# Performance work log

Hardware: AMD Instinct MI355X
Metric: run time of the kernel (lower is better)

The kernel has to match this reference:

```python
import jax, jax.numpy as jnp
import numpy as np

NUM_HEADS = 16
ROPE_BASE = 10000.0
MAX_POS = 4096


def _rope_tables(head_dim):
    inv_freq = 1.0 / (ROPE_BASE ** (np.arange(0, head_dim, 2, dtype=np.float32) / head_dim))
    freqs = np.arange(MAX_POS, dtype=np.float32)[:, None] * inv_freq[None, :]
    emb = np.concatenate([freqs, freqs], axis=-1)  # [MAX_POS, head_dim]
    return jnp.asarray(np.cos(emb)), jnp.asarray(np.sin(emb))


def _rotate_half(x):
    d = x.shape[-1] // 2
    return jnp.concatenate([-x[..., d:], x[..., :d]], axis=-1)


def _apply_rope(x, pos, cos_t, sin_t):
    # x: [B,H,S,D], pos: [B,S]
    cos = cos_t[pos][:, None]  # [B,1,S,D]
    sin = sin_t[pos][:, None]
    return x * cos + _rotate_half(x) * sin


def setup_inputs() -> dict:
    key = jax.random.key(0)
    ks = jax.random.split(key, 8)
    B, N, M, C = 2, 2048, 2048, 1024
    s = 1.0 / np.sqrt(C)
    return {
        "query": jax.random.normal(ks[0], (B, N, C), jnp.float32),
        "key": jax.random.normal(ks[1], (B, M, C), jnp.float32),
        "query_pos": jnp.broadcast_to(jnp.arange(N, dtype=jnp.int32), (B, N)),
        "key_pos": jnp.broadcast_to(jnp.arange(M, dtype=jnp.int32), (B, M)),
        "Wq": jax.random.normal(ks[2], (C, C), jnp.float32) * s,
        "bq": jnp.zeros((C,), jnp.float32),
        "Wk": jax.random.normal(ks[3], (C, C), jnp.float32) * s,
        "Wv": jax.random.normal(ks[4], (C, C), jnp.float32) * s,
        "bv": jnp.zeros((C,), jnp.float32),
        "Wo": jax.random.normal(ks[5], (C, C), jnp.float32) * s,
        "bo": jnp.zeros((C,), jnp.float32),
    }


def reference(query, key, query_pos, key_pos, Wq, bq, Wk, Wv, bv, Wo, bo):
    B, N, C = query.shape
    M = key.shape[1]
    H = NUM_HEADS
    D = C // H
    scale = D ** -0.5
    cos_t, sin_t = _rope_tables(D)

    value = key  # value defaults to key
    identity = query

    q = (query @ Wq.T + bq).reshape(B, N, H, D).transpose(0, 2, 1, 3)
    k = (key @ Wk.T).reshape(B, M, H, D).transpose(0, 2, 1, 3)
    v = (value @ Wv.T + bv).reshape(B, M, H, D).transpose(0, 2, 1, 3)

    q = _apply_rope(q, query_pos, cos_t, sin_t)
    k = _apply_rope(k, key_pos, cos_t, sin_t)

    attn = jnp.einsum('bhnd,bhmd->bhnm', q, k) * scale
    attn = jax.nn.softmax(attn, axis=-1)
    x = jnp.einsum('bhnm,bhmd->bhnd', attn, v)  # [B,H,N,D]
    x = x.transpose(0, 2, 1, 3).reshape(B, N, C)
    x = x @ Wo.T + bo
    return x + identity
```

## Files before the change

### kernel.cpp

```cpp
#include <hip/hip_runtime.h>
#include <hip/hip_bf16.h>
#include <stdint.h>

#define B_ 2
#define N_ 2048
#define M_ 2048
#define C_ 1024
#define H_ 16
#define D_ 64

typedef __attribute__((ext_vector_type(8))) short s16x8;
typedef __attribute__((ext_vector_type(4))) short s16x4;
typedef __attribute__((ext_vector_type(4))) float f32x4;
typedef __attribute__((ext_vector_type(16))) float f32x16;

__device__ __attribute__((always_inline)) inline short f2b(float f){
    __hip_bfloat16 h = __float2bfloat16(f); short s; __builtin_memcpy(&s, &h, 2); return s;
}
__device__ __attribute__((always_inline)) inline float b2f(short s){
    __hip_bfloat16 h; __builtin_memcpy(&h, &s, 2); return __bfloat162float(h);
}

#define MFMA16(a,b,c) __builtin_amdgcn_mfma_f32_16x16x32_bf16(a,b,c,0,0,0)
#define MFMA32(a,b,c) __builtin_amdgcn_mfma_f32_32x32x16_bf16(a,b,c,0,0,0)

__device__ __attribute__((always_inline)) inline void gl_lds16(const void* g, void* l){
    __builtin_amdgcn_global_load_lds((__attribute__((address_space(1))) void*)g,
                                     (__attribute__((address_space(3))) void*)l, 16, 0, 0);
}
__device__ __attribute__((always_inline)) inline unsigned fbits(float f){
    unsigned u; __builtin_memcpy(&u, &f, 4); return u;
}

__global__ void cvt_all(const float* __restrict__ q, const float* __restrict__ k,
                        const float* __restrict__ wq, const float* __restrict__ wk,
                        const float* __restrict__ wv, const float* __restrict__ wo,
                        short* __restrict__ dst){
    long i = ((long)blockIdx.x * 256 + threadIdx.x) * 8;
    const float* src; long off;
    if      (i <  4194304L){ src = q;  off = i; }
    else if (i <  8388608L){ src = k;  off = i - 4194304L; }
    else if (i <  9437184L){ src = wq; off = i - 8388608L; }
    else if (i < 10485760L){ src = wk; off = i - 9437184L; }
    else if (i < 11534336L){ src = wv; off = i - 10485760L; }
    else                   { src = wo; off = i - 11534336L; }
    float4 a = *(const float4*)(src + off);
    float4 b = *(const float4*)(src + off + 4);
    s16x8 o;
    o[0]=f2b(a.x); o[1]=f2b(a.y); o[2]=f2b(a.z); o[3]=f2b(a.w);
    o[4]=f2b(b.x); o[5]=f2b(b.y); o[6]=f2b(b.z); o[7]=f2b(b.w);
    *(s16x8*)(dst + i) = o;
}

__global__ __launch_bounds__(256, 3) void gemm_qkv(
    const short* __restrict__ qbf, const short* __restrict__ kbf,
    const short* __restrict__ W,
    const float* __restrict__ bq, const float* __restrict__ bv,
    short* __restrict__ qproj, short* __restrict__ kproj, short* __restrict__ vT)
{
    __shared__ short As[128 * 32];
    __shared__ short Bs[128 * 32];
    const int n0 = blockIdx.x * 128, m0 = blockIdx.y * 128;
    const int sel = n0 >> 10;
    const short* A = (sel == 0) ? qbf : kbf;
    const int tid = threadIdx.x, lane = tid & 63, wave = tid >> 6;
    const int quad = lane >> 4, l16 = lane & 15;
    const int wr = (wave >> 1) * 64, wc = (wave & 1) * 64;
    const int srow = lane >> 2, scol = (lane & 3) * 8;

    f32x4 acc[4][4] = {};

    const short* Ag = A + (size_t)(m0 + wave * 32 + srow) * C_ + scol;
    const short* Bg = W + (size_t)(n0 + wave * 32 + srow) * C_ + scol;
    short* lA0 = As + (wave * 32) * 32;
    short* lA1 = As + (wave * 32 + 16) * 32;
    short* lB0 = Bs + (wave * 32) * 32;
    short* lB1 = Bs + (wave * 32 + 16) * 32;

    for (int k0 = 0; k0 < C_; k0 += 32){
        __syncthreads();
        gl_lds16(Ag + k0, lA0);
        gl_lds16(Ag + k0 + 16 * (size_t)C_, lA1);
        gl_lds16(Bg + k0, lB0);
        gl_lds16(Bg + k0 + 16 * (size_t)C_, lB1);
        __syncthreads();
        s16x8 af[4], bfr[4];
        #pragma unroll
        for (int t = 0; t < 4; t++) af[t]  = *(const s16x8*)&As[(wr + t*16 + l16) * 32 + quad * 8];
        #pragma unroll
        for (int t = 0; t < 4; t++) bfr[t] = *(const s16x8*)&Bs[(wc + t*16 + l16) * 32 + quad * 8];
        #pragma unroll
        for (int i = 0; i < 4; i++)
            #pragma unroll
            for (int j = 0; j < 4; j++)
                acc[i][j] = MFMA16(af[i], bfr[j], acc[i][j]);
    }

    if (sel <= 1){
        short* dst = sel ? kproj : qproj;
        const float* bp = sel ? nullptr : bq;
        const int coff = sel << 10;
        #pragma unroll
        for (int j = 0; j < 4; j++){
            int c = n0 + wc + j * 16 + l16 - coff;
            float bb = bp ? bp[c] : 0.0f;
            #pragma unroll
            for (int i = 0; i < 4; i++){
                int row = m0 + wr + i * 16 + quad * 4;
                #pragma unroll
                for (int r = 0; r < 4; r++)
                    dst[(size_t)(row + r) * C_ + c] = f2b(acc[i][j][r] + bb);
            }
        }
    } else {
        #pragma unroll
        for (int j = 0; j < 4; j++){
            int col = n0 - 2048 + wc + j * 16 + l16;
            int h = col >> 6, d = col & 63;
            float bb = bv[col];
            #pragma unroll
            for (int i = 0; i < 4; i++){
                int row = m0 + wr + i * 16 + quad * 4;
                int b = row >> 11, m = row & 2047;
                unsigned u0 = (unsigned)(unsigned short)f2b(acc[i][j][0] + bb) |
                              ((unsigned)(unsigned short)f2b(acc[i][j][1] + bb) << 16);
                unsigned u1 = (unsigned)(unsigned short)f2b(acc[i][j][2] + bb) |
                              ((unsigned)(unsigned short)f2b(acc[i][j][3] + bb) << 16);
                uint2 u; u.x = u0; u.y = u1;
                *(uint2*)&vT[(((size_t)(b * H_ + h)) * D_ + d) * M_ + m] = u;
            }
        }
    }
}

__global__ __launch_bounds__(256, 4) void gemm_out(
    const short* __restrict__ A, const short* __restrict__ W,
    const float* __restrict__ bias, const float* __restrict__ resid,
    float* __restrict__ outf)
{
    __shared__ short As[128 * 32];
    __shared__ short Bs[64 * 32];
    const int n0 = blockIdx.x * 64, m0 = blockIdx.y * 128;
    const int tid = threadIdx.x, lane = tid & 63, wave = tid >> 6;
    const int quad = lane >> 4, l16 = lane & 15;
    const int srow = lane >> 2, scol = (lane & 3) * 8;

    f32x4 acc[2][4] = {};
    const short* Ag = A + (size_t)(m0 + wave * 32 + srow) * C_ + scol;
    const short* Bg = W + (size_t)(n0 + wave * 16 + srow) * C_ + scol;
    short* lA0 = As + (wave * 32) * 32;
    short* lA1 = As + (wave * 32 + 16) * 32;
    short* lB  = Bs + (wave * 16) * 32;

    for (int k0 = 0; k0 < C_; k0 += 32){
        __syncthreads();
        gl_lds16(Ag + k0, lA0);
        gl_lds16(Ag + k0 + 16 * (size_t)C_, lA1);
        gl_lds16(Bg + k0, lB);
        __syncthreads();
        s16x8 af[2], bfr[4];
        #pragma unroll
        for (int t = 0; t < 2; t++) af[t]  = *(const s16x8*)&As[(wave*32 + t*16 + l16) * 32 + quad * 8];
        #pragma unroll
        for (int t = 0; t < 4; t++) bfr[t] = *(const s16x8*)&Bs[(t*16 + l16) * 32 + quad * 8];
        #pragma unroll
        for (int i = 0; i < 2; i++)
            #pragma unroll
            for (int j = 0; j < 4; j++)
                acc[i][j] = MFMA16(af[i], bfr[j], acc[i][j]);
    }

    #pragma unroll
    for (int j = 0; j < 4; j++){
        int c = n0 + j * 16 + l16;
        float bb = bias[c];
        #pragma unroll
        for (int i = 0; i < 2; i++){
            int row = m0 + wave * 32 + i * 16 + quad * 4;
            #pragma unroll
            for (int r = 0; r < 4; r++){
                size_t idx = (size_t)(row + r) * C_ + c;
                outf[idx] = acc[i][j][r] + bb + resid[idx];
            }
        }
    }
}

__global__ void rope_k(short* __restrict__ k, const int* __restrict__ kpos){
    int t = blockIdx.x * blockDim.x + threadIdx.x;
    int i = t & 31;
    int h = (t >> 5) & (H_ - 1);
    int row = t >> 9;
    int pos = kpos[row];
    short* base = k + (size_t)row * C_ + h * D_;
    float x1 = b2f(base[i]), x2 = b2f(base[i + 32]);
    float invf = exp2f((float)i * (-13.287712379549449f / 32.0f));
    float f = (float)pos * invf;
    float c = __cosf(f), s = __sinf(f);
    base[i]      = f2b(x1 * c - x2 * s);
    base[i + 32] = f2b(x2 * c + x1 * s);
}

__global__ __launch_bounds__(256, 2) void flash_attn(
    const short* __restrict__ q, const short* __restrict__ k,
    const short* __restrict__ vt, short* __restrict__ o,
    const int* __restrict__ qpos)
{
    __shared__ short smem[27136];
    const int b = blockIdx.y >> 4, h = blockIdx.y & 15;
    const int n0 = blockIdx.x * 128;
    const int tid = threadIdx.x, lane = tid & 63, wave = tid >> 6;
    const int hi = lane >> 5, l32 = lane & 31;
    const int wq = wave & 1, kq = wave >> 1;

    s16x8 qf[2][4];
    const float fac = 0.18033688011112042f;
    #pragma unroll
    for (int qt = 0; qt < 2; qt++){
        int qrow = n0 + wq * 64 + qt * 32 + l32;
        const short* qg = &q[((size_t)(b * N_ + qrow)) * C_ + h * D_];
        float pos = (float)qpos[b * N_ + qrow];
        s16x8 raw[4];
        #pragma unroll
        for (int c = 0; c < 4; c++) raw[c] = *(const s16x8*)&qg[c * 16 + hi * 8];
        #pragma unroll
        for (int c = 0; c < 2; c++){
            s16x8 olo, ohi8;
            #pragma unroll
            for (int j = 0; j < 8; j++){
                int irot = c * 16 + hi * 8 + j;
                float invf = exp2f((float)irot * (-13.287712379549449f / 32.0f));
                float ang = pos * invf;
                float cs = __cosf(ang), sn = __sinf(ang);
                float x1 = b2f(raw[c][j]), x2 = b2f(raw[c + 2][j]);
                olo[j]  = f2b((x1 * cs - x2 * sn) * fac);
                ohi8[j] = f2b((x2 * cs + x1 * sn) * fac);
            }
            qf[qt][c] = olo; qf[qt][c + 2] = ohi8;
        }
    }

    const short* kg = k  + (size_t)(b * M_) * C_ + h * D_;
    const short* vg = vt + ((size_t)(b * H_ + h)) * D_ * M_;
    const int srow0 = tid >> 3, sseg = (tid & 7) * 8;

    union V8 { s16x8 v; uint2 u[2]; };
    V8 kreg[2], vreg[2];

    #pragma unroll
    for (int ii = 0; ii < 2; ii++){
        int row = srow0 + 32 * ii;
        kreg[ii].v = *(const s16x8*)&kg[(size_t)row * C_ + sseg];
        vreg[ii].v = *(const s16x8*)&vg[(size_t)row * M_ + sseg];
    }
    #pragma unroll
    for (int ii = 0; ii < 2; ii++){
        int row = srow0 + 32 * ii;
        short* kd = &smem[row * 68 + sseg];
        *(uint2*)kd = kreg[ii].u[0]; *(uint2*)(kd + 4) = kreg[ii].u[1];
        short* vd = &smem[8704 + row * 68 + sseg];
        *(uint2*)vd = vreg[ii].u[0]; *(uint2*)(vd + 4) = vreg[ii].u[1];
    }

    f32x16 zero16 = {};
    f32x16 oacc[2][2] = {zero16, zero16, zero16, zero16};
    float lacc[2] = {0.f, 0.f};
    short* Pw = &smem[17408 + wave * 2304];

    for (int st = 0; st < 32; st++){
        const int p = st & 1;
        __syncthreads();
        if (st < 31){
            #pragma unroll
            for (int ii = 0; ii < 2; ii++){
                int row = srow0 + 32 * ii;
                kreg[ii].v = *(const s16x8*)&kg[((size_t)((st + 1) * 64 + row)) * C_ + sseg];
                vreg[ii].v = *(const s16x8*)&vg[(size_t)row * M_ + (st + 1) * 64 + sseg];
            }
        }
        const short* Kp = &smem[p * 4352];
        const short* Vp = &smem[8704 + p * 4352];

        s16x4 kf[4][2];
        #pragma unroll
        for (int c = 0; c < 4; c++){
            const short* a = &Kp[(kq * 32 + l32) * 68 + c * 16 + hi * 8];
            kf[c][0] = *(const s16x4*)a; kf[c][1] = *(const s16x4*)(a + 4);
        }
        #pragma unroll
        for (int qt = 0; qt < 2; qt++){
            f32x16 sv = {};
            #pragma unroll
            for (int c = 0; c < 4; c++){
                s16x8 ka = __builtin_shufflevector(kf[c][0], kf[c][1], 0,1,2,3,4,5,6,7);
                sv = MFMA32(ka, qf[qt][c], sv);
            }
            float ls = 0.f;
            unsigned pb[8];
            #pragma unroll
            for (int g = 0; g < 4; g++){
                float p0 = __builtin_amdgcn_exp2f(sv[4*g+0]);
                float p1 = __builtin_amdgcn_exp2f(sv[4*g+1]);
                float p2 = __builtin_amdgcn_exp2f(sv[4*g+2]);
                float p3 = __builtin_amdgcn_exp2f(sv[4*g+3]);
                ls += (p0 + p1) + (p2 + p3);
                pb[2*g]   = __builtin_amdgcn_perm(fbits(p1), fbits(p0), 0x07060302);
                pb[2*g+1] = __builtin_amdgcn_perm(fbits(p3), fbits(p2), 0x07060302);
            }
            lacc[qt] += ls;
            #pragma unroll
            for (int g = 0; g < 4; g++){
                short* d = &Pw[(qt * 32 + l32) * 36 + 8 * g + 4 * hi];
                uint2 u; u.x = pb[2*g]; u.y = pb[2*g+1];
                *(uint2*)d = u;
            }
        }
        asm volatile("s_waitcnt lgkmcnt(0)" ::: "memory");

        s16x8 pf[2][2], vf[2][2];
        #pragma unroll
        for (int qt = 0; qt < 2; qt++)
            #pragma unroll
            for (int c = 0; c < 2; c++){
                const short* a = &Pw[(qt * 32 + l32) * 36 + c * 16 + hi * 8];
                pf[qt][c] = __builtin_shufflevector(*(const s16x4*)a, *(const s16x4*)(a + 4),
                                                    0,1,2,3,4,5,6,7);
            }
        #pragma unroll
        for (int dt = 0; dt < 2; dt++)
            #pragma unroll
            for (int c = 0; c < 2; c++){
                const short* a = &Vp[(dt * 32 + l32) * 68 + kq * 32 + c * 16 + hi * 8];
                vf[dt][c] = __builtin_shufflevector(*(const s16x4*)a, *(const s16x4*)(a + 4),
                                                    0,1,2,3,4,5,6,7);
            }
        #pragma unroll
        for (int qt = 0; qt < 2; qt++)
            #pragma unroll
            for (int dt = 0; dt < 2; dt++)
                #pragma unroll
                for (int c = 0; c < 2; c++)
                    oacc[qt][dt] = MFMA32(pf[qt][c], vf[dt][c], oacc[qt][dt]);

        __syncthreads();
        if (st < 31){
            int pn = p ^ 1;
            #pragma unroll
            for (int ii = 0; ii < 2; ii++){
                int row = srow0 + 32 * ii;
                short* kd = &smem[pn * 4352 + row * 68 + sseg];
                *(uint2*)kd = kreg[ii].u[0]; *(uint2*)(kd + 4) = kreg[ii].u[1];
                short* vd = &smem[8704 + pn * 4352 + row * 68 + sseg];
                *(uint2*)vd = vreg[ii].u[0]; *(uint2*)(vd + 4) = vreg[ii].u[1];
            }
        }
    }

    __syncthreads();

    float* LO   = (float*)smem;
    float* Lsum = (float*)&smem[26624];
    float* Linv = Lsum + 128;

    float l0[2];
    #pragma unroll
    for (int qt = 0; qt < 2; qt++)
        l0[qt] = lacc[qt] + __shfl_xor(lacc[qt], 32);

    if (kq == 1){
        #pragma unroll
        for (int qt = 0; qt < 2; qt++)
            Lsum[wq * 64 + qt * 32 + l32] = l0[qt];
        #pragma unroll
        for (int qt = 0; qt < 2; qt++)
            #pragma unroll
            for (int dt = 0; dt < 2; dt++)
                #pragma unroll
                for (int e = 0; e < 16; e++){
                    int qrow = wq * 64 + qt * 32 + (e & 3) + 8 * (e >> 2) + 4 * hi;
                    LO[qrow * 65 + dt * 32 + l32] = oacc[qt][dt][e];
                }
    }
    __syncthreads();
    if (kq == 0){
        #pragma unroll
        for (int qt = 0; qt < 2; qt++){
            float lt = l0[qt] + Lsum[wq * 64 + qt * 32 + l32];
            Linv[wq * 64 + qt * 32 + l32] = 1.0f / lt;
        }
        asm volatile("s_waitcnt lgkmcnt(0)" ::: "memory");
        #pragma unroll
        for (int qt = 0; qt < 2; qt++)
            #pragma unroll
            for (int dt = 0; dt < 2; dt++)
                #pragma unroll
                for (int e = 0; e < 16; e++){
                    int qrow = wq * 64 + qt * 32 + (e & 3) + 8 * (e >> 2) + 4 * hi;
                    float val = (oacc[qt][dt][e] + LO[qrow * 65 + dt * 32 + l32]) * Linv[qrow];
                    o[((size_t)(b * N_ + n0 + qrow)) * C_ + h * D_ + dt * 32 + l32] = f2b(val);
                }
    }
}

extern "C" void kernel_launch(void* const* d_in, const int* in_sizes, int n_in,
                              void* d_out, int out_size, void* d_ws, size_t ws_size,
                              hipStream_t stream) {
    const float* query = (const float*)d_in[0];
    const float* key   = (const float*)d_in[1];
    const int*   qpos  = (const int*)d_in[2];
    const int*   kpos  = (const int*)d_in[3];
    const float* Wq    = (const float*)d_in[4];
    const float* bq    = (const float*)d_in[5];
    const float* Wk    = (const float*)d_in[6];
    const float* Wv    = (const float*)d_in[7];
    const float* bv    = (const float*)d_in[8];
    const float* Wo    = (const float*)d_in[9];
    const float* bo    = (const float*)d_in[10];
    float* out = (float*)d_out;

    const size_t E4M = (size_t)4 * 1024 * 1024;
    const size_t E1M = (size_t)1024 * 1024;
    short* ws    = (short*)d_ws;
    short* qbf   = ws;
    short* kbf   = qbf   + E4M;
    short* wqkvb = kbf   + E4M;
    short* wob   = wqkvb + 3 * E1M;
    short* qproj = wob   + E1M;
    short* kproj = qproj + E4M;
    short* vT    = kproj + E4M;
    short* attn  = qbf;

    cvt_all<<<6144, 256, 0, stream>>>(query, key, Wq, Wk, Wv, Wo, ws);

    gemm_qkv<<<dim3(24, 32), 256, 0, stream>>>(qbf, kbf, wqkvb, bq, bv,
                                               qproj, kproj, vT);

    rope_k<<<(B_ * M_ * H_ * 32) / 256, 256, 0, stream>>>(kproj, kpos);

    flash_attn<<<dim3(16, 32), 256, 0, stream>>>(qproj, kproj, vT, attn, qpos);

    gemm_out<<<dim3(16, 32), 256, 0, stream>>>(attn, wob, bo, query, out);
}
```

Before: 215.8 us.

## Repack softmax probabilities in registers via permlane32 swap instead of LDS

The attention loop now converts the exponentiated scores to bf16 with v_cvt_pk_bf16_f32 and rearranges them into the PV MFMA operand layout using v_permlane32_swap, instead of writing P to shared memory and reading it back. This drops the per-wave P staging buffer, which shrinks shared memory use, and removes one __syncthreads per tile iteration because the barrier at the top of the loop already orders reuse of the K/V buffers. It also switches the bf16 conversion from truncation to rounded packing. The cost is reliance on gfx950-specific inline asm and a somewhat different rounding of P.

```diff
diff --git a/kernel.cpp b/kernel.cpp
--- a/kernel.cpp
+++ b/kernel.cpp
@@ -30,6 +30,14 @@
 }
 __device__ __attribute__((always_inline)) inline unsigned fbits(float f){
     unsigned u; __builtin_memcpy(&u, &f, 4); return u;
+}
+__device__ __attribute__((always_inline)) inline unsigned cvtpk(float lo, float hi){
+    unsigned r;
+    asm("v_cvt_pk_bf16_f32 %0, %1, %2" : "=v"(r) : "v"(lo), "v"(hi));
+    return r;
+}
+__device__ __attribute__((always_inline)) inline void lane32swap(unsigned &a, unsigned &b){
+    asm("v_permlane32_swap_b32 %0, %1" : "+v"(a), "+v"(b));
 }
 
 __global__ void cvt_all(const float* __restrict__ q, const float* __restrict__ k,
@@ -206,7 +214,7 @@
     const short* __restrict__ vt, short* __restrict__ o,
     const int* __restrict__ qpos)
 {
-    __shared__ short smem[27136];
+    __shared__ short smem[17920];
     const int b = blockIdx.y >> 4, h = blockIdx.y & 15;
     const int n0 = blockIdx.x * 128;
     const int tid = threadIdx.x, lane = tid & 63, wave = tid >> 6;
@@ -265,7 +273,6 @@
     f32x16 zero16 = {};
     f32x16 oacc[2][2] = {zero16, zero16, zero16, zero16};
     float lacc[2] = {0.f, 0.f};
-    short* Pw = &smem[17408 + wave * 2304];
 
     for (int st = 0; st < 32; st++){
         const int p = st & 1;
@@ -287,45 +294,7 @@
             const short* a = &Kp[(kq * 32 + l32) * 68 + c * 16 + hi * 8];
             kf[c][0] = *(const s16x4*)a; kf[c][1] = *(const s16x4*)(a + 4);
         }
-        #pragma unroll
-        for (int qt = 0; qt < 2; qt++){
-            f32x16 sv = {};
-            #pragma unroll
-            for (int c = 0; c < 4; c++){
-                s16x8 ka = __builtin_shufflevector(kf[c][0], kf[c][1], 0,1,2,3,4,5,6,7);
-                sv = MFMA32(ka, qf[qt][c], sv);
-            }
-            float ls = 0.f;
-            unsigned pb[8];
-            #pragma unroll
-            for (int g = 0; g < 4; g++){
-                float p0 = __builtin_amdgcn_exp2f(sv[4*g+0]);
-                float p1 = __builtin_amdgcn_exp2f(sv[4*g+1]);
-                float p2 = __builtin_amdgcn_exp2f(sv[4*g+2]);
-                float p3 = __builtin_amdgcn_exp2f(sv[4*g+3]);
-                ls += (p0 + p1) + (p2 + p3);
-                pb[2*g]   = __builtin_amdgcn_perm(fbits(p1), fbits(p0), 0x07060302);
-                pb[2*g+1] = __builtin_amdgcn_perm(fbits(p3), fbits(p2), 0x07060302);
-            }
-            lacc[qt] += ls;
-            #pragma unroll
-            for (int g = 0; g < 4; g++){
-                short* d = &Pw[(qt * 32 + l32) * 36 + 8 * g + 4 * hi];
-                uint2 u; u.x = pb[2*g]; u.y = pb[2*g+1];
-                *(uint2*)d = u;
-            }
-        }
-        asm volatile("s_waitcnt lgkmcnt(0)" ::: "memory");
-
-        s16x8 pf[2][2], vf[2][2];
-        #pragma unroll
-        for (int qt = 0; qt < 2; qt++)
-            #pragma unroll
-            for (int c = 0; c < 2; c++){
-                const short* a = &Pw[(qt * 32 + l32) * 36 + c * 16 + hi * 8];
-                pf[qt][c] = __builtin_shufflevector(*(const s16x4*)a, *(const s16x4*)(a + 4),
-                                                    0,1,2,3,4,5,6,7);
-            }
+        s16x8 vf[2][2];
         #pragma unroll
         for (int dt = 0; dt < 2; dt++)
             #pragma unroll
@@ -334,6 +303,37 @@
                 vf[dt][c] = __builtin_shufflevector(*(const s16x4*)a, *(const s16x4*)(a + 4),
                                                     0,1,2,3,4,5,6,7);
             }
+
+        s16x8 pf[2][2];
+        #pragma unroll
+        for (int qt = 0; qt < 2; qt++){
+            f32x16 sv = {};
+            #pragma unroll
+            for (int c = 0; c < 4; c++){
+                s16x8 ka = __builtin_shufflevector(kf[c][0], kf[c][1], 0,1,2,3,4,5,6,7);
+                sv = MFMA32(ka, qf[qt][c], sv);
+            }
+            float pe[16];
+            #pragma unroll
+            for (int e = 0; e < 16; e++) pe[e] = __builtin_amdgcn_exp2f(sv[e]);
+            float ls = 0.f;
+            #pragma unroll
+            for (int e = 0; e < 16; e += 4) ls += (pe[e] + pe[e+1]) + (pe[e+2] + pe[e+3]);
+            lacc[qt] += ls;
+            #pragma unroll
+            for (int c = 0; c < 2; c++){
+                unsigned a1 = cvtpk(pe[8*c + 0], pe[8*c + 1]);
+                unsigned a2 = cvtpk(pe[8*c + 2], pe[8*c + 3]);
+                unsigned b1 = cvtpk(pe[8*c + 4], pe[8*c + 5]);
+                unsigned b2 = cvtpk(pe[8*c + 6], pe[8*c + 7]);
+                lane32swap(a1, b1);
+                lane32swap(a2, b2);
+                union { unsigned u[4]; s16x8 v; } pk;
+                pk.u[0] = a1; pk.u[1] = a2; pk.u[2] = b1; pk.u[3] = b2;
+                pf[qt][c] = pk.v;
+            }
+        }
+
         #pragma unroll
         for (int qt = 0; qt < 2; qt++)
             #pragma unroll
@@ -342,7 +342,6 @@
                 for (int c = 0; c < 2; c++)
                     oacc[qt][dt] = MFMA32(pf[qt][c], vf[dt][c], oacc[qt][dt]);
 
-        __syncthreads();
         if (st < 31){
             int pn = p ^ 1;
             #pragma unroll
@@ -359,7 +358,7 @@
     __syncthreads();
 
     float* LO   = (float*)smem;
-    float* Lsum = (float*)&smem[26624];
+    float* Lsum = (float*)&smem[17408];
     float* Linv = Lsum + 128;
 
     float l0[2];
```

Measured after the change: 210.8 us. 2.3% less time.
